# Kernel optimization log

Hardware: AMD Instinct MI355X
Metric: run time of the kernel (lower is better)

## Reference

```python
import jax, jax.numpy as jnp
import numpy as np

B, N, C = 2, 4096, 768
H = 12  # num_heads; head_dim = C // H = 64


def setup_inputs() -> dict:
    key = jax.random.key(0)
    kx, kq, kk, kv = jax.random.split(key, 4)
    s = C ** -0.5  # keep param magnitudes sane
    return {
        "x": jax.random.normal(kx, (B, N, C), dtype=jnp.float32),
        "Wq": jax.random.normal(kq, (C, C), dtype=jnp.float32) * s,
        "Wk": jax.random.normal(kk, (C, C), dtype=jnp.float32) * s,
        "Wv": jax.random.normal(kv, (C, C), dtype=jnp.float32) * s,  # created but UNUSED, as in original
    }


def reference(x, Wq, Wk, Wv):
    b, n, c = x.shape
    hd = c // H
    # torch nn.Linear: y = x @ W.T
    q = (x @ Wq.T).reshape(b, n, H, hd).transpose(0, 2, 1, 3)  # [B,H,N,hd]
    k = (x @ Wk.T).reshape(b, n, H, hd).transpose(0, 2, 1, 3)
    # BUG preserved from source: value path uses the K projection, Wv is unused
    v = (x @ Wk.T).reshape(b, n, H, hd).transpose(0, 2, 1, 3)
    # scale by full C (not head_dim), as in source
    attn = jnp.einsum("bhqd,bhkd->bhqk", q, k) * (c ** -0.5)
    attn = jax.nn.softmax(attn, axis=-1)
    out = jnp.einsum("bhqk,bhkd->bhqd", attn, v)  # [B,H,N,hd]
    return out.transpose(0, 2, 1, 3).reshape(b, n, c)
```

## Files before the change

### kernel.cpp

```cpp
#include <hip/hip_runtime.h>

typedef __bf16 bf16;
typedef __bf16 bf16x4 __attribute__((ext_vector_type(4)));
typedef __bf16 bf16x8 __attribute__((ext_vector_type(8)));
typedef float  f32x4  __attribute__((ext_vector_type(4)));
typedef int    int4v  __attribute__((ext_vector_type(4)));

#define NTOK 4096
#define NH   12
#define HD   64
#define CDIM 768

#define K2SCALE 0.05205928442089389f

#define MFMA __builtin_amdgcn_mfma_f32_16x16x32_bf16

__device__ __forceinline__ bf16* swz(bf16* base, int row, int byteoff) {
  return (bf16*)((char*)base + row * 128 +
                 ((((byteoff >> 4) ^ (row & 7)) << 4) | (byteoff & 15)));
}
__device__ __forceinline__ const bf16* swz(const bf16* base, int row, int byteoff) {
  return (const bf16*)((const char*)base + row * 128 +
                 ((((byteoff >> 4) ^ (row & 7)) << 4) | (byteoff & 15)));
}

__global__ __launch_bounds__(256) void cast_kernel(
    const float* __restrict__ x, const float* __restrict__ wq, const float* __restrict__ wk,
    bf16* __restrict__ xb, bf16* __restrict__ wqb, bf16* __restrict__ wkb,
    long nx, long nw) {
  long i4 = ((long)blockIdx.x * 256 + threadIdx.x) * 4;
  if (i4 >= nx + 2 * nw) return;
  const float* src; bf16* dst;
  if (i4 < nx)            { src = x  + i4;            dst = xb  + i4; }
  else if (i4 < nx + nw)  { src = wq + (i4 - nx);     dst = wqb + (i4 - nx); }
  else                    { src = wk + (i4 - nx - nw); dst = wkb + (i4 - nx - nw); }
  f32x4 v = *(const f32x4*)src;
  *(bf16x4*)dst = __builtin_convertvector(v, bf16x4);
}

__global__ __launch_bounds__(256) void proj_kernel(
    const bf16* __restrict__ xb, const bf16* __restrict__ wqb, const bf16* __restrict__ wkb,
    bf16* __restrict__ Qb, bf16* __restrict__ Kb) {
  __shared__ __align__(16) bf16 Ap[128 * 64];
  __shared__ __align__(16) bf16 Bp[128 * 64];
  const int tid = threadIdx.x;
  const int w = tid >> 6, lane = tid & 63, l15 = lane & 15, quad = lane >> 4;
  const int m0 = blockIdx.x * 128;
  const int j0 = blockIdx.y * 128;
  const bf16* W   = blockIdx.z ? wkb : wqb;
  bf16*       Out = blockIdx.z ? Kb  : Qb;
  const float oscale = blockIdx.z ? 1.0f : K2SCALE;

  const int srow = tid >> 3, scb = (tid & 7) * 16, soff = (tid & 7) * 8;
  const bf16* pa = xb + (long)(m0 + srow) * CDIM + soff;
  const bf16* pb = W  + (long)(j0 + srow) * CDIM + soff;

  f32x4 acc[2][8] = {};
  int4v rA[4], rB[4];
#pragma unroll
  for (int i = 0; i < 4; ++i) {
    rA[i] = *(const int4v*)(pa + (long)i * 32 * CDIM);
    rB[i] = *(const int4v*)(pb + (long)i * 32 * CDIM);
  }

  for (int kt = 0; kt < CDIM / 64; ++kt) {
    __syncthreads();
#pragma unroll
    for (int i = 0; i < 4; ++i) {
      *(int4v*)swz(Ap, srow + i * 32, scb) = rA[i];
      *(int4v*)swz(Bp, srow + i * 32, scb) = rB[i];
    }
    __syncthreads();
    const long koff = (long)((kt == CDIM / 64 - 1) ? kt : kt + 1) * 64;
#pragma unroll
    for (int i = 0; i < 4; ++i) {
      rA[i] = *(const int4v*)(pa + (long)i * 32 * CDIM + koff);
      rB[i] = *(const int4v*)(pb + (long)i * 32 * CDIM + koff);
    }
#pragma unroll
    for (int kk = 0; kk < 2; ++kk) {
      bf16x8 a[2], b[8];
#pragma unroll
      for (int rt = 0; rt < 2; ++rt)
        a[rt] = *(const bf16x8*)swz(Ap, w * 32 + rt * 16 + l15, kk * 64 + quad * 16);
#pragma unroll
      for (int ct = 0; ct < 8; ++ct)
        b[ct] = *(const bf16x8*)swz(Bp, ct * 16 + l15, kk * 64 + quad * 16);
#pragma unroll
      for (int rt = 0; rt < 2; ++rt)
#pragma unroll
        for (int ct = 0; ct < 8; ++ct)
          acc[rt][ct] = MFMA(a[rt], b[ct], acc[rt][ct], 0, 0, 0);
    }
  }
#pragma unroll
  for (int rt = 0; rt < 2; ++rt)
#pragma unroll
    for (int ct = 0; ct < 8; ++ct)
#pragma unroll
      for (int reg = 0; reg < 4; ++reg) {
        int m = m0 + w * 32 + rt * 16 + quad * 4 + reg;
        int j = j0 + ct * 16 + l15;
        int b = m >> 12, n = m & (NTOK - 1);
        int h = j >> 6, d = j & (HD - 1);
        Out[(((long)(b * NH + h) * NTOK + n) << 6) + d] = (bf16)(acc[rt][ct][reg] * oscale);
      }
}

__global__ __launch_bounds__(256) void transpose_kernel(
    const bf16* __restrict__ Kb, bf16* __restrict__ Ktb) {
  __shared__ __align__(16) bf16 T[64 * 72];
  const int tid = threadIdx.x;
  const int n0 = blockIdx.x * 64;
  const long bh = blockIdx.y;
#pragma unroll
  for (int i = 0; i < 2; ++i) {
    int c = tid + i * 256;
    int row = c >> 3, off = (c & 7) * 8;
    bf16x8 v = *(const bf16x8*)(Kb + ((bh << 12) + n0 + row) * HD + off);
#pragma unroll
    for (int e = 0; e < 8; ++e) T[(off + e) * 72 + row] = v[e];
  }
  __syncthreads();
#pragma unroll
  for (int i = 0; i < 2; ++i) {
    int c = tid + i * 256;
    int d = c >> 3, koff = (c & 7) * 8;
    int4v v = *(const int4v*)(&T[d * 72 + koff]);
    *(int4v*)(Ktb + ((bh << 6) + d) * (long)NTOK + n0 + koff) = v;
  }
}


#define QKT(SX, MT, KC)                                                        \
  {                                                                            \
    bf16x8 a0 = *(const bf16x8*)swz(KC, (MT) * 16 + l15, quad * 16);           \
    bf16x8 a1 = *(const bf16x8*)swz(KC, (MT) * 16 + l15, 64 + quad * 16);      \
    SX[0] = MFMA(a0, bq[0][0], SX[0], 0, 0, 0);                                \
    SX[1] = MFMA(a0, bq[1][0], SX[1], 0, 0, 0);                                \
    SX[0] = MFMA(a1, bq[0][1], SX[0], 0, 0, 0);                                \
    SX[1] = MFMA(a1, bq[1][1], SX[1], 0, 0, 0);                                \
  }

#define EXP2P(SX, MT)                                                          \
  {                                                                            \
    f32x4 p0, p1;                                                              \
    _Pragma("unroll") for (int r = 0; r < 4; ++r) {                            \
      p0[r] = __builtin_amdgcn_exp2f(SX[0][r]);                                \
      p1[r] = __builtin_amdgcn_exp2f(SX[1][r]);                                \
    }                                                                          \
    lacc[0] += (p0[0] + p0[1]) + (p0[2] + p0[3]);                              \
    lacc[1] += (p1[0] + p1[1]) + (p1[2] + p1[3]);                              \
    *(bf16x4*)swz(QP, w * 32 + l15, (MT) * 32 + quad * 8) =                    \
        __builtin_convertvector(p0, bf16x4);                                   \
    *(bf16x4*)swz(QP, w * 32 + 16 + l15, (MT) * 32 + quad * 8) =               \
        __builtin_convertvector(p1, bf16x4);                                   \
  }

#define PVKK(KK, KTC)                                                          \
  {                                                                            \
    bf16x8 bp0 = *(const bf16x8*)swz(QP, w * 32 + l15, (KK) * 64 + quad * 16); \
    bf16x8 bp1 = *(const bf16x8*)swz(QP, w * 32 + 16 + l15, (KK) * 64 + quad * 16); \
    _Pragma("unroll") for (int mt = 0; mt < 4; ++mt) {                         \
      bf16x8 av = *(const bf16x8*)swz(KTC, mt * 16 + l15, (KK) * 64 + quad * 16); \
      o[mt][0] = MFMA(av, bp0, o[mt][0], 0, 0, 0);                             \
      o[mt][1] = MFMA(av, bp1, o[mt][1], 0, 0, 0);                             \
    }                                                                          \
  }

#define HALF_ITER(C, WK, WT, PK_, PT_, T2)                                     \
  {                                                                            \
    const bf16* Kc  = Ks  + (C) * 4096;                                        \
    const bf16* KTc = Kts + (C) * 4096;                                        \
    bf16* KcW  = Ks  + (1 - (C)) * 4096;                                       \
    bf16* KTcW = Kts + (1 - (C)) * 4096;                                       \
    f32x4 s0[2] = {}, s1[2] = {}, s2[2] = {}, s3[2] = {};                      \
    __builtin_amdgcn_s_setprio(1);                                             \
    QKT(s0, 0, Kc)                                                             \
    QKT(s1, 1, Kc)                                                             \
    *(int4v*)swz(KcW, srow, scb) = WK[0];                                      \
    *(int4v*)swz(KcW, srow + 32, scb) = WK[1];                                 \
    EXP2P(s0, 0)                                                               \
    QKT(s2, 2, Kc)                                                             \
    *(int4v*)swz(KTcW, srow, scb) = WT[0];                                     \
    *(int4v*)swz(KTcW, srow + 32, scb) = WT[1];                                \
    EXP2P(s1, 1)                                                               \
    QKT(s3, 3, Kc)                                                             \
    { const long ko = (long)(T2) * 64;                                         \
      PK_[0] = *(const int4v*)(pk + ko * HD);                                  \
      PK_[1] = *(const int4v*)(pk + (ko + 32) * HD);                           \
      PT_[0] = *(const int4v*)(pkt + ko);                                      \
      PT_[1] = *(const int4v*)(pkt + ko + 32L * NTOK); }                       \
    EXP2P(s2, 2)                                                               \
    EXP2P(s3, 3)                                                               \
    PVKK(0, KTc)                                                               \
    PVKK(1, KTc)                                                               \
    __builtin_amdgcn_s_setprio(0);                                             \
    __syncthreads();                                                           \
  }

__global__ __launch_bounds__(256, 3) void attn_kernel(
    const bf16* __restrict__ Qb, const bf16* __restrict__ Kb, const bf16* __restrict__ Ktb,
    float* __restrict__ out) {
  __shared__ __align__(16) bf16 QP[128 * 64];
  __shared__ __align__(16) bf16 Ks[2 * 64 * 64];
  __shared__ __align__(16) bf16 Kts[2 * 64 * 64];

  const int tid = threadIdx.x;
  const int w = tid >> 6, lane = tid & 63, l15 = lane & 15, quad = lane >> 4;
  const int q0 = blockIdx.x * 128;
  const int bh = blockIdx.y;
  const int b = bh / NH, h = bh % NH;
  const bf16* Qhead  = Qb  + (long)bh * NTOK * HD;
  const bf16* Khead  = Kb  + (long)bh * NTOK * HD;
  const bf16* Kthead = Ktb + (long)bh * HD * NTOK;

  const int srow = tid >> 3, scb = (tid & 7) * 16, soff = (tid & 7) * 8;
  const bf16* pk  = Khead  + (long)srow * HD + soff;
  const bf16* pkt = Kthead + (long)srow * NTOK + soff;

#pragma unroll
  for (int i = 0; i < 4; ++i) {
    int c = tid + i * 256;
    int row = c >> 3, cb = (c & 7) * 16;
    int4v v = *(const int4v*)(Qhead + (long)(q0 + row) * HD + (c & 7) * 8);
    *(int4v*)swz(QP, row, cb) = v;
  }

  int4v rAK[2], rAT[2], rBK[2], rBT[2];
  rAK[0] = *(const int4v*)(pk);
  rAK[1] = *(const int4v*)(pk + 32 * HD);
  rAT[0] = *(const int4v*)(pkt);
  rAT[1] = *(const int4v*)(pkt + 32L * NTOK);
  rBK[0] = *(const int4v*)(pk + 64 * HD);
  rBK[1] = *(const int4v*)(pk + 96 * HD);
  rBT[0] = *(const int4v*)(pkt + 64);
  rBT[1] = *(const int4v*)(pkt + 64 + 32L * NTOK);
  *(int4v*)swz(Ks, srow, scb)       = rAK[0];
  *(int4v*)swz(Ks, srow + 32, scb)  = rAK[1];
  *(int4v*)swz(Kts, srow, scb)      = rAT[0];
  *(int4v*)swz(Kts, srow + 32, scb) = rAT[1];
  __syncthreads();

  bf16x8 bq[2][2];
#pragma unroll
  for (int nt = 0; nt < 2; ++nt)
#pragma unroll
    for (int kk = 0; kk < 2; ++kk)
      bq[nt][kk] = *(const bf16x8*)swz(QP, w * 32 + nt * 16 + l15, kk * 64 + quad * 16);

  f32x4 o[4][2] = {};
  float lacc[2] = {0.f, 0.f};

  for (int t = 0; t < NTOK / 64; t += 2) {
    const int n2a = (t + 2 < NTOK / 64) ? t + 2 : NTOK / 64 - 1;
    const int n2b = (t + 3 < NTOK / 64) ? t + 3 : NTOK / 64 - 1;
    HALF_ITER(0, rBK, rBT, rAK, rAT, n2a)
    HALF_ITER(1, rAK, rAT, rBK, rBT, n2b)
  }

#pragma unroll
  for (int nt = 0; nt < 2; ++nt) {
    float l = lacc[nt];
    l += __shfl_xor(l, 16, 64);
    l += __shfl_xor(l, 32, 64);
    float rl = 1.0f / l;
    int n = q0 + w * 32 + nt * 16 + l15;
#pragma unroll
    for (int mt = 0; mt < 4; ++mt) {
      f32x4 v;
#pragma unroll
      for (int reg = 0; reg < 4; ++reg) v[reg] = o[mt][nt][reg] * rl;
      *(f32x4*)(&out[((long)(b * NTOK + n)) * CDIM + h * HD + mt * 16 + quad * 4]) = v;
    }
  }
}

extern "C" void kernel_launch(void* const* d_in, const int* in_sizes, int n_in,
                              void* d_out, int out_size, void* d_ws, size_t ws_size,
                              hipStream_t stream) {
  const float* x  = (const float*)d_in[0];
  const float* Wq = (const float*)d_in[1];
  const float* Wk = (const float*)d_in[2];
  float* out = (float*)d_out;
  char* ws = (char*)d_ws;

  const long NX = (long)2 * NTOK * CDIM;
  const long NW = (long)CDIM * CDIM;

  bf16* xb  = (bf16*)(ws);
  bf16* Ktb = (bf16*)(ws);
  bf16* wqb = (bf16*)(ws + NX * 2);
  bf16* wkb = (bf16*)(ws + NX * 2 + NW * 2);
  bf16* Qb  = (bf16*)(ws + NX * 2 + NW * 4);
  bf16* Kb  = (bf16*)(ws + NX * 2 + NW * 4 + NX * 2);

  long tot4 = (NX + 2 * NW) / 4;
  cast_kernel<<<dim3((tot4 + 255) / 256), 256, 0, stream>>>(x, Wq, Wk, xb, wqb, wkb, NX, NW);
  proj_kernel<<<dim3(8192 / 128, CDIM / 128, 2), 256, 0, stream>>>(xb, wqb, wkb, Qb, Kb);
  transpose_kernel<<<dim3(NTOK / 64, 2 * NH), 256, 0, stream>>>(Kb, Ktb);
  attn_kernel<<<dim3(NTOK / 128, 2 * NH), 256, 0, stream>>>(Qb, Kb, Ktb, out);
}
```

Baseline: 228.7 us.

## Shrink attention query tile to 64 and load transposed K straight into registers

The attention kernel now processes 64 queries per block (16 per wave) instead of 128, which halves the per-wave accumulators and Q fragments. It drops the shared-memory staging buffer for transposed K and has each lane load its PV-MFMA operands directly from global memory. It also raises the occupancy hint to 4 blocks per CU and remaps a 1-D grid so that blocks sharing a head are spread across (b,h). The cost is that each K/K^T tile is reused by half as many queries, so global and L2 traffic for K roughly doubles, and uncoalesced direct global loads for K^T sit on the critical path.

```diff
diff --git a/kernel.cpp b/kernel.cpp
--- a/kernel.cpp
+++ b/kernel.cpp
@@ -136,45 +136,37 @@
   {                                                                            \
     bf16x8 a0 = *(const bf16x8*)swz(KC, (MT) * 16 + l15, quad * 16);           \
     bf16x8 a1 = *(const bf16x8*)swz(KC, (MT) * 16 + l15, 64 + quad * 16);      \
-    SX[0] = MFMA(a0, bq[0][0], SX[0], 0, 0, 0);                                \
-    SX[1] = MFMA(a0, bq[1][0], SX[1], 0, 0, 0);                                \
-    SX[0] = MFMA(a1, bq[0][1], SX[0], 0, 0, 0);                                \
-    SX[1] = MFMA(a1, bq[1][1], SX[1], 0, 0, 0);                                \
+    SX = MFMA(a0, bq[0], SX, 0, 0, 0);                                         \
+    SX = MFMA(a1, bq[1], SX, 0, 0, 0);                                         \
   }
 
 #define EXP2P(SX, MT)                                                          \
   {                                                                            \
-    f32x4 p0, p1;                                                              \
-    _Pragma("unroll") for (int r = 0; r < 4; ++r) {                            \
-      p0[r] = __builtin_amdgcn_exp2f(SX[0][r]);                                \
-      p1[r] = __builtin_amdgcn_exp2f(SX[1][r]);                                \
-    }                                                                          \
-    lacc[0] += (p0[0] + p0[1]) + (p0[2] + p0[3]);                              \
-    lacc[1] += (p1[0] + p1[1]) + (p1[2] + p1[3]);                              \
-    *(bf16x4*)swz(QP, w * 32 + l15, (MT) * 32 + quad * 8) =                    \
-        __builtin_convertvector(p0, bf16x4);                                   \
-    *(bf16x4*)swz(QP, w * 32 + 16 + l15, (MT) * 32 + quad * 8) =               \
-        __builtin_convertvector(p1, bf16x4);                                   \
-  }
-
-#define PVKK(KK, KTC)                                                          \
-  {                                                                            \
-    bf16x8 bp0 = *(const bf16x8*)swz(QP, w * 32 + l15, (KK) * 64 + quad * 16); \
-    bf16x8 bp1 = *(const bf16x8*)swz(QP, w * 32 + 16 + l15, (KK) * 64 + quad * 16); \
-    _Pragma("unroll") for (int mt = 0; mt < 4; ++mt) {                         \
-      bf16x8 av = *(const bf16x8*)swz(KTC, mt * 16 + l15, (KK) * 64 + quad * 16); \
-      o[mt][0] = MFMA(av, bp0, o[mt][0], 0, 0, 0);                             \
-      o[mt][1] = MFMA(av, bp1, o[mt][1], 0, 0, 0);                             \
-    }                                                                          \
-  }
-
-#define HALF_ITER(C, WK, WT, PK_, PT_, T2)                                     \
-  {                                                                            \
-    const bf16* Kc  = Ks  + (C) * 4096;                                        \
-    const bf16* KTc = Kts + (C) * 4096;                                        \
-    bf16* KcW  = Ks  + (1 - (C)) * 4096;                                       \
-    bf16* KTcW = Kts + (1 - (C)) * 4096;                                       \
-    f32x4 s0[2] = {}, s1[2] = {}, s2[2] = {}, s3[2] = {};                      \
+    f32x4 p;                                                                   \
+    _Pragma("unroll") for (int r = 0; r < 4; ++r)                              \
+        p[r] = __builtin_amdgcn_exp2f(SX[r]);                                  \
+    lacc += (p[0] + p[1]) + (p[2] + p[3]);                                     \
+    *(bf16x4*)swz(QP, w * 16 + l15, (MT) * 32 + quad * 8) =                    \
+        __builtin_convertvector(p, bf16x4);                                    \
+  }
+
+#define PVKK(KK)                                                               \
+  {                                                                            \
+    bf16x8 bp = *(const bf16x8*)swz(QP, w * 16 + l15, (KK) * 64 + quad * 16);  \
+    _Pragma("unroll") for (int mt = 0; mt < 4; ++mt)                           \
+        o[mt] = MFMA(av[mt][KK], bp, o[mt], 0, 0, 0);                          \
+  }
+
+#define HALF_ITER(C, WK, PK_, TC, T2)                                          \
+  {                                                                            \
+    const bf16* Kc = Ks + (C) * 4096;                                          \
+    bf16* KcW = Ks + (1 - (C)) * 4096;                                         \
+    bf16x8 av[4][2];                                                           \
+    const bf16* ta = pav + (long)(TC) * 64;                                    \
+    _Pragma("unroll") for (int mt = 0; mt < 4; ++mt)                           \
+      _Pragma("unroll") for (int kk = 0; kk < 2; ++kk)                         \
+        av[mt][kk] = *(const bf16x8*)(ta + (long)mt * 16 * NTOK + kk * 32);    \
+    f32x4 s0 = {}, s1 = {}, s2 = {}, s3 = {};                                  \
     __builtin_amdgcn_s_setprio(1);                                             \
     QKT(s0, 0, Kc)                                                             \
     QKT(s1, 1, Kc)                                                             \
@@ -182,34 +174,31 @@
     *(int4v*)swz(KcW, srow + 32, scb) = WK[1];                                 \
     EXP2P(s0, 0)                                                               \
     QKT(s2, 2, Kc)                                                             \
-    *(int4v*)swz(KTcW, srow, scb) = WT[0];                                     \
-    *(int4v*)swz(KTcW, srow + 32, scb) = WT[1];                                \
+    { const bf16* gp = pk + (long)(T2) * 64 * HD;                              \
+      PK_[0] = *(const int4v*)gp;                                              \
+      PK_[1] = *(const int4v*)(gp + 32 * HD); }                                \
     EXP2P(s1, 1)                                                               \
     QKT(s3, 3, Kc)                                                             \
-    { const long ko = (long)(T2) * 64;                                         \
-      PK_[0] = *(const int4v*)(pk + ko * HD);                                  \
-      PK_[1] = *(const int4v*)(pk + (ko + 32) * HD);                           \
-      PT_[0] = *(const int4v*)(pkt + ko);                                      \
-      PT_[1] = *(const int4v*)(pkt + ko + 32L * NTOK); }                       \
     EXP2P(s2, 2)                                                               \
     EXP2P(s3, 3)                                                               \
-    PVKK(0, KTc)                                                               \
-    PVKK(1, KTc)                                                               \
+    PVKK(0)                                                                    \
+    PVKK(1)                                                                    \
     __builtin_amdgcn_s_setprio(0);                                             \
     __syncthreads();                                                           \
   }
 
-__global__ __launch_bounds__(256, 3) void attn_kernel(
+__global__ __launch_bounds__(256, 4) void attn_kernel(
     const bf16* __restrict__ Qb, const bf16* __restrict__ Kb, const bf16* __restrict__ Ktb,
     float* __restrict__ out) {
-  __shared__ __align__(16) bf16 QP[128 * 64];
+  __shared__ __align__(16) bf16 QP[64 * 64];
   __shared__ __align__(16) bf16 Ks[2 * 64 * 64];
-  __shared__ __align__(16) bf16 Kts[2 * 64 * 64];
 
   const int tid = threadIdx.x;
   const int w = tid >> 6, lane = tid & 63, l15 = lane & 15, quad = lane >> 4;
-  const int q0 = blockIdx.x * 128;
-  const int bh = blockIdx.y;
+  const int g = blockIdx.x;
+  const int r = g % 24;
+  const int q0 = (g / 24) * 64;
+  const int bh = (r & 7) * 3 + (r >> 3);
   const int b = bh / NH, h = bh % NH;
   const bf16* Qhead  = Qb  + (long)bh * NTOK * HD;
   const bf16* Khead  = Kb  + (long)bh * NTOK * HD;
@@ -217,60 +206,51 @@
 
   const int srow = tid >> 3, scb = (tid & 7) * 16, soff = (tid & 7) * 8;
   const bf16* pk  = Khead  + (long)srow * HD + soff;
-  const bf16* pkt = Kthead + (long)srow * NTOK + soff;
-
-#pragma unroll
-  for (int i = 0; i < 4; ++i) {
+  const bf16* pav = Kthead + (long)l15 * NTOK + quad * 8;
+
+#pragma unroll
+  for (int i = 0; i < 2; ++i) {
     int c = tid + i * 256;
     int row = c >> 3, cb = (c & 7) * 16;
     int4v v = *(const int4v*)(Qhead + (long)(q0 + row) * HD + (c & 7) * 8);
     *(int4v*)swz(QP, row, cb) = v;
   }
 
-  int4v rAK[2], rAT[2], rBK[2], rBT[2];
+  int4v rAK[2], rBK[2];
   rAK[0] = *(const int4v*)(pk);
   rAK[1] = *(const int4v*)(pk + 32 * HD);
-  rAT[0] = *(const int4v*)(pkt);
-  rAT[1] = *(const int4v*)(pkt + 32L * NTOK);
   rBK[0] = *(const int4v*)(pk + 64 * HD);
   rBK[1] = *(const int4v*)(pk + 96 * HD);
-  rBT[0] = *(const int4v*)(pkt + 64);
-  rBT[1] = *(const int4v*)(pkt + 64 + 32L * NTOK);
-  *(int4v*)swz(Ks, srow, scb)       = rAK[0];
-  *(int4v*)swz(Ks, srow + 32, scb)  = rAK[1];
-  *(int4v*)swz(Kts, srow, scb)      = rAT[0];
-  *(int4v*)swz(Kts, srow + 32, scb) = rAT[1];
+  *(int4v*)swz(Ks, srow, scb)      = rAK[0];
+  *(int4v*)swz(Ks, srow + 32, scb) = rAK[1];
   __syncthreads();
 
-  bf16x8 bq[2][2];
-#pragma unroll
-  for (int nt = 0; nt < 2; ++nt)
-#pragma unroll
-    for (int kk = 0; kk < 2; ++kk)
-      bq[nt][kk] = *(const bf16x8*)swz(QP, w * 32 + nt * 16 + l15, kk * 64 + quad * 16);
-
-  f32x4 o[4][2] = {};
-  float lacc[2] = {0.f, 0.f};
+  bf16x8 bq[2];
+#pragma unroll
+  for (int kk = 0; kk < 2; ++kk)
+    bq[kk] = *(const bf16x8*)swz(QP, w * 16 + l15, kk * 64 + quad * 16);
+
+  f32x4 o[4] = {};
+  float lacc = 0.f;
 
   for (int t = 0; t < NTOK / 64; t += 2) {
     const int n2a = (t + 2 < NTOK / 64) ? t + 2 : NTOK / 64 - 1;
     const int n2b = (t + 3 < NTOK / 64) ? t + 3 : NTOK / 64 - 1;
-    HALF_ITER(0, rBK, rBT, rAK, rAT, n2a)
-    HALF_ITER(1, rAK, rAT, rBK, rBT, n2b)
-  }
-
-#pragma unroll
-  for (int nt = 0; nt < 2; ++nt) {
-    float l = lacc[nt];
+    HALF_ITER(0, rBK, rAK, t, n2a)
+    HALF_ITER(1, rAK, rBK, t + 1, n2b)
+  }
+
+  {
+    float l = lacc;
     l += __shfl_xor(l, 16, 64);
     l += __shfl_xor(l, 32, 64);
     float rl = 1.0f / l;
-    int n = q0 + w * 32 + nt * 16 + l15;
+    int n = q0 + w * 16 + l15;
 #pragma unroll
     for (int mt = 0; mt < 4; ++mt) {
       f32x4 v;
 #pragma unroll
-      for (int reg = 0; reg < 4; ++reg) v[reg] = o[mt][nt][reg] * rl;
+      for (int reg = 0; reg < 4; ++reg) v[reg] = o[mt][reg] * rl;
       *(f32x4*)(&out[((long)(b * NTOK + n)) * CDIM + h * HD + mt * 16 + quad * 4]) = v;
     }
   }
@@ -299,5 +279,5 @@
   cast_kernel<<<dim3((tot4 + 255) / 256), 256, 0, stream>>>(x, Wq, Wk, xb, wqb, wkb, NX, NW);
   proj_kernel<<<dim3(8192 / 128, CDIM / 128, 2), 256, 0, stream>>>(xb, wqb, wkb, Qb, Kb);
   transpose_kernel<<<dim3(NTOK / 64, 2 * NH), 256, 0, stream>>>(Kb, Ktb);
-  attn_kernel<<<dim3(NTOK / 128, 2 * NH), 256, 0, stream>>>(Qb, Kb, Ktb, out);
-}
+  attn_kernel<<<dim3((NTOK / 64) * 2 * NH), 256, 0, stream>>>(Qb, Kb, Ktb, out);
+}
```

Result: slower. 471.3 us (+106.1%).
